# Optimization experiments

Hardware: AMD Instinct MI355X
Metric: run time of the kernel (lower is better)

The kernel has to match this reference:

```python
import jax, jax.numpy as jnp
import numpy as np
import math

NUM_HEADS = 16
D_MODEL = 1024
HEAD_DIM = D_MODEL // NUM_HEADS


def setup_inputs() -> dict:
    key = jax.random.key(0)
    k1, k2, k3 = jax.random.split(key, 3)
    x = jax.random.normal(k1, (4, 2048, D_MODEL), dtype=jnp.float32)
    # Linear(d_model, 3*d_model, bias=False): y = x @ w_qkv, w_qkv: [d_model, 3*d_model]
    w_qkv = jax.random.normal(k2, (D_MODEL, 3 * D_MODEL), dtype=jnp.float32) * (1.0 / math.sqrt(D_MODEL))
    w_o = jax.random.normal(k3, (D_MODEL, D_MODEL), dtype=jnp.float32) * (1.0 / math.sqrt(D_MODEL))
    return {"x": x, "w_qkv": w_qkv, "w_o": w_o}


def reference(x, w_qkv, w_o):
    B, S, _ = x.shape
    H, Dh = NUM_HEADS, HEAD_DIM
    qkv = (x @ w_qkv).reshape(B, S, 3, H, Dh)
    q = qkv[:, :, 0].transpose(0, 2, 1, 3)  # [B, H, S, Dh]
    k = qkv[:, :, 1].transpose(0, 2, 1, 3)
    v = qkv[:, :, 2].transpose(0, 2, 1, 3)
    scale = 1.0 / math.sqrt(Dh + 1e-9)
    scores = jnp.einsum("bhqd,bhkd->bhqk", q, k) * scale  # [B, H, S, S]
    probs = jax.nn.softmax(scores, axis=-1)
    # dropout is identity in eval mode
    out = jnp.einsum("bhqk,bhkd->bhqd", probs, v)  # [B, H, S, Dh]
    out = out.transpose(0, 2, 1, 3).reshape(B, S, H * Dh)
    return out @ w_o
```

## Files before the change

kernel.cpp:

```cpp
#include <hip/hip_runtime.h>
#include <hip/hip_bf16.h>

typedef __bf16 bf16_t;
typedef __bf16 bf16x8 __attribute__((ext_vector_type(8)));
typedef float f32x4 __attribute__((ext_vector_type(4)));
typedef unsigned int uint32x2 __attribute__((ext_vector_type(2)));
typedef unsigned int uint32x4 __attribute__((ext_vector_type(4)));

#define B_SZ 4
#define SEQ 2048
#define NH 16
#define DH 64
#define DM 1024
#define RSQ (3 * DM)

__device__ __forceinline__ void gload_lds16(const bf16_t* g, bf16_t* l) {
  __builtin_amdgcn_global_load_lds(
      (const __attribute__((address_space(1))) unsigned int*)g,
      (__attribute__((address_space(3))) unsigned int*)l, 16, 0, 0);
}

__device__ __forceinline__ unsigned lds_b32addr(void* p) {
  return (unsigned)(uintptr_t)(__attribute__((address_space(3))) void*)p;
}

__global__ __launch_bounds__(256) void f32_to_bf16_kernel(
    const float* __restrict__ in, bf16_t* __restrict__ out, int n) {
  int i = (blockIdx.x * blockDim.x + threadIdx.x) * 4;
  if (i >= n) return;
  float4 v = *reinterpret_cast<const float4*>(in + i);
  bf16_t o[4] = {(bf16_t)v.x, (bf16_t)v.y, (bf16_t)v.z, (bf16_t)v.w};
  *reinterpret_cast<uint2*>(out + i) = *reinterpret_cast<const uint2*>(o);
}

__global__ __launch_bounds__(256) void transpose_f32_bf16_kernel(
    const float* __restrict__ in, bf16_t* __restrict__ outT, int K, int N,
    int scale_cols, float scale) {
  __shared__ float tile[32][33];
  const int tx = threadIdx.x & 31;
  const int ty = threadIdx.x >> 5;
  const int n0 = blockIdx.x * 32;
  const int k0 = blockIdx.y * 32;
#pragma unroll
  for (int j = 0; j < 4; ++j)
    tile[ty + j * 8][tx] = in[(size_t)(k0 + ty + j * 8) * N + n0 + tx];
  __syncthreads();
#pragma unroll
  for (int j = 0; j < 4; ++j) {
    int n = n0 + ty + j * 8;
    float s = (n < scale_cols) ? scale : 1.0f;
    outT[(size_t)n * K + k0 + tx] = (bf16_t)(tile[tx][ty + j * 8] * s);
  }
}

template <typename OutT>
__global__ __launch_bounds__(512, 2) void gemm8p_kernel(
    const bf16_t* __restrict__ A, const bf16_t* __restrict__ Bt,
    OutT* __restrict__ C, int M, int N, int K, int NB) {
  __shared__ __align__(16) bf16_t As[2][128 * 64];
  __shared__ __align__(16) bf16_t Bs[2][256 * 64];

  const int tid = threadIdx.x;
  const int lane = tid & 63;
  const int wid = tid >> 6;
  const int l16 = lane & 15;
  const int g4 = lane >> 4;
  const int wm = wid >> 2;
  const int wn = wid & 3;
  const int tiles = K >> 6;

  const int nwg = gridDim.x;
  const int bid = blockIdx.x;
  const int swz = (bid & 7) * (nwg >> 3) + (bid >> 3);
  const int m0 = (swz / NB) * 128;
  const int n0 = (swz % NB) * 256;

  const bf16_t* aglob = A + (size_t)(m0 + (tid >> 3)) * K + (tid & 7) * 8;

  auto stageA = [&](int t) {
    int tt = (t == tiles) ? 0 : t;
    int k0 = tt * 64;
    int buf = tt & 1;
#pragma unroll
    for (int i = 0; i < 2; ++i)
      gload_lds16(aglob + (size_t)i * 64 * K + k0,
                  &As[buf][i * 4096 + wid * 512]);
  };
  auto stageB = [&](int t, int h) {
    int tt = (t == tiles) ? 0 : t;
    int k0 = tt * 64;
    int buf = tt & 1;
#pragma unroll
    for (int j = 0; j < 2; ++j) {
      int wrow = (2 * j + (wid >> 2)) * 64 + (wid & 3) * 8 + h * 32;
      gload_lds16(
          Bt + (size_t)(n0 + wrow + (lane >> 3)) * K + k0 + (lane & 7) * 8,
          &Bs[buf][wrow * 64]);
    }
  };

  f32x4 acc[4][4] = {};

  stageA(0);
  stageB(0, 0);
  stageB(0, 1);
  asm volatile("s_waitcnt vmcnt(2)" ::: "memory");
  __builtin_amdgcn_s_barrier();
  __builtin_amdgcn_sched_barrier(0);

#pragma unroll 2
  for (int t = 0; t < tiles; ++t) {
    const int buf = t & 1;
    const int abase = (wm * 64 + l16) * 64 + g4 * 8;
    const int bbase = (wn * 64 + l16) * 64 + g4 * 8;

    bf16x8 af[4][2], bf[2][2];
#pragma unroll
    for (int m = 0; m < 4; ++m)
#pragma unroll
      for (int ks = 0; ks < 2; ++ks)
        af[m][ks] = *reinterpret_cast<const bf16x8*>(
            &As[buf][abase + m * 16 * 64 + ks * 32]);
#pragma unroll
    for (int n = 0; n < 2; ++n)
#pragma unroll
      for (int ks = 0; ks < 2; ++ks)
        bf[n][ks] = *reinterpret_cast<const bf16x8*>(
            &Bs[buf][bbase + n * 16 * 64 + ks * 32]);

    stageA(t + 1);
    stageB(t + 1, 0);
    asm volatile("s_waitcnt vmcnt(4)" ::: "memory");
    __builtin_amdgcn_s_barrier();
    __builtin_amdgcn_sched_barrier(0);

    __builtin_amdgcn_s_setprio(1);
#pragma unroll
    for (int m = 0; m < 4; ++m)
#pragma unroll
      for (int n = 0; n < 2; ++n)
#pragma unroll
        for (int ks = 0; ks < 2; ++ks)
          acc[m][n] = __builtin_amdgcn_mfma_f32_16x16x32_bf16(
              af[m][ks], bf[n][ks], acc[m][n], 0, 0, 0);
    __builtin_amdgcn_s_setprio(0);
    __builtin_amdgcn_s_barrier();
    __builtin_amdgcn_sched_barrier(0);

    bf16x8 bg[2][2];
#pragma unroll
    for (int n = 0; n < 2; ++n)
#pragma unroll
      for (int ks = 0; ks < 2; ++ks)
        bg[n][ks] = *reinterpret_cast<const bf16x8*>(
            &Bs[buf][bbase + (n + 2) * 16 * 64 + ks * 32]);

    stageB(t + 1, 1);
    asm volatile("s_waitcnt vmcnt(2)" ::: "memory");
    __builtin_amdgcn_s_barrier();
    __builtin_amdgcn_sched_barrier(0);

    __builtin_amdgcn_s_setprio(1);
#pragma unroll
    for (int m = 0; m < 4; ++m)
#pragma unroll
      for (int n = 0; n < 2; ++n)
#pragma unroll
        for (int ks = 0; ks < 2; ++ks)
          acc[m][n + 2] = __builtin_amdgcn_mfma_f32_16x16x32_bf16(
              af[m][ks], bg[n][ks], acc[m][n + 2], 0, 0, 0);
    __builtin_amdgcn_s_setprio(0);
    __builtin_amdgcn_s_barrier();
    __builtin_amdgcn_sched_barrier(0);
  }

  asm volatile("s_waitcnt vmcnt(0)" ::: "memory");

#pragma unroll
  for (int m = 0; m < 4; ++m)
#pragma unroll
    for (int n = 0; n < 4; ++n)
#pragma unroll
      for (int r = 0; r < 4; ++r) {
        int row = m0 + wm * 64 + m * 16 + g4 * 4 + r;
        int col = n0 + wn * 64 + n * 16 + l16;
        C[(size_t)row * N + col] = (OutT)acc[m][n][r];
      }
}

template <bool PRE>
__device__ __forceinline__ void attn_body(
    const bf16_t* kp, const bf16_t* vp_next, bf16_t* vst_next, unsigned vrd,
    const bf16x8 (&qf)[4][2], f32x4 (&acc_o)[16], float (&lsum)[4]) {
  uint32x4 kf[2][2];
#pragma unroll
  for (int half = 0; half < 2; ++half)
#pragma unroll
    for (int kh = 0; kh < 2; ++kh)
      asm volatile("global_load_dwordx4 %0, %1, off"
                   : "=v"(kf[half][kh])
                   : "v"(kp + (size_t)half * 64 * RSQ + kh * 32)
                   : "memory");

  if constexpr (PRE) {
#pragma unroll
    for (int t = 0; t < 4; ++t)
      gload_lds16(vp_next + t * 16, vst_next + t * 512);
  }

  if constexpr (PRE)
    asm volatile("s_waitcnt vmcnt(8)" ::: "memory");
  else
    asm volatile("s_waitcnt vmcnt(4)" ::: "memory");

  uint32x2 vr[4][2];
#define TRR(dst, OFFSTR)                              \
  asm volatile("ds_read_b64_tr_b16 %0, %1 offset:" OFFSTR \
               : "=v"(dst)                            \
               : "v"(vrd))
  TRR(vr[0][0], "0");    TRR(vr[0][1], "512");
  TRR(vr[1][0], "1024"); TRR(vr[1][1], "1536");
  TRR(vr[2][0], "2048"); TRR(vr[2][1], "2560");
  TRR(vr[3][0], "3072"); TRR(vr[3][1], "3584");
#undef TRR

  if constexpr (PRE)
    asm volatile("s_waitcnt vmcnt(4)" ::: "memory");
  else
    asm volatile("s_waitcnt vmcnt(0)" ::: "memory");
  __builtin_amdgcn_sched_barrier(0);

  f32x4 sA[4] = {}, sB[4] = {};
#pragma unroll
  for (int qb = 0; qb < 4; ++qb) {
    sA[qb] = __builtin_amdgcn_mfma_f32_16x16x32_bf16(
        __builtin_bit_cast(bf16x8, kf[0][0]), qf[qb][0], sA[qb], 0, 0, 0);
    sA[qb] = __builtin_amdgcn_mfma_f32_16x16x32_bf16(
        __builtin_bit_cast(bf16x8, kf[0][1]), qf[qb][1], sA[qb], 0, 0, 0);
    sB[qb] = __builtin_amdgcn_mfma_f32_16x16x32_bf16(
        __builtin_bit_cast(bf16x8, kf[1][0]), qf[qb][0], sB[qb], 0, 0, 0);
    sB[qb] = __builtin_amdgcn_mfma_f32_16x16x32_bf16(
        __builtin_bit_cast(bf16x8, kf[1][1]), qf[qb][1], sB[qb], 0, 0, 0);
  }

  bf16x8 pf[4];
#pragma unroll
  for (int qb = 0; qb < 4; ++qb) {
    float p0 = __builtin_amdgcn_exp2f(sA[qb][0]);
    float p1 = __builtin_amdgcn_exp2f(sA[qb][1]);
    float p2 = __builtin_amdgcn_exp2f(sA[qb][2]);
    float p3 = __builtin_amdgcn_exp2f(sA[qb][3]);
    float p4 = __builtin_amdgcn_exp2f(sB[qb][0]);
    float p5 = __builtin_amdgcn_exp2f(sB[qb][1]);
    float p6 = __builtin_amdgcn_exp2f(sB[qb][2]);
    float p7 = __builtin_amdgcn_exp2f(sB[qb][3]);
    lsum[qb] += ((p0 + p1) + (p2 + p3)) + ((p4 + p5) + (p6 + p7));
    pf[qb][0] = (bf16_t)p0; pf[qb][1] = (bf16_t)p1;
    pf[qb][2] = (bf16_t)p2; pf[qb][3] = (bf16_t)p3;
    pf[qb][4] = (bf16_t)p4; pf[qb][5] = (bf16_t)p5;
    pf[qb][6] = (bf16_t)p6; pf[qb][7] = (bf16_t)p7;
  }

  asm volatile("s_waitcnt lgkmcnt(0)" ::: "memory");
  __builtin_amdgcn_sched_barrier(0);
  bf16x8 vf[4];
#pragma unroll
  for (int db = 0; db < 4; ++db) {
    uint32x4 c = {vr[db][0].x, vr[db][0].y, vr[db][1].x, vr[db][1].y};
    vf[db] = __builtin_bit_cast(bf16x8, c);
  }
#pragma unroll
  for (int qb = 0; qb < 4; ++qb)
#pragma unroll
    for (int db = 0; db < 4; ++db)
      acc_o[qb * 4 + db] = __builtin_amdgcn_mfma_f32_16x16x32_bf16(
          pf[qb], vf[db], acc_o[qb * 4 + db], 0, 0, 0);
}

__global__ __launch_bounds__(256) void attn_kernel(
    const bf16_t* __restrict__ qkv, bf16_t* __restrict__ out) {
  __shared__ __align__(16) unsigned char smem[33792];
  bf16_t* Vlds = (bf16_t*)smem;
  float(*Obuf)[66] = (float(*)[66])smem;
  float* lbuf = (float*)(smem + 32768);

  const int tid = threadIdx.x;
  const int lane = tid & 63;
  const int wid = tid >> 6;
  const int l16 = lane & 15;
  const int g4 = lane >> 4;

  const int D = blockIdx.x;
  const int g = ((D >> 8) << 3) + (D & 7);
  const int h = g & 15;
  const int b = g >> 4;
  const int q0 = ((D >> 3) & 31) * 64;

  const size_t base = (size_t)b * SEQ * RSQ;

  bf16x8 qf[4][2];
#pragma unroll
  for (int qb = 0; qb < 4; ++qb)
#pragma unroll
    for (int kh = 0; kh < 2; ++kh)
      qf[qb][kh] = __builtin_bit_cast(
          bf16x8, *reinterpret_cast<const uint4*>(
                      qkv + base + (size_t)(q0 + qb * 16 + l16) * RSQ + h * DH +
                      kh * 32 + g4 * 8));

  const bf16_t* kbase =
      qkv + base + (size_t)(wid * 16 + l16) * RSQ + DM + h * DH + g4 * 8;

  const int keyoff = ((lane >> 5) << 6) + wid * 16 + (((lane >> 3) & 3) << 2) +
                     ((lane >> 1) & 3);
  const bf16_t* vsrc =
      qkv + base + (size_t)keyoff * RSQ + 2 * DM + h * DH + (lane & 1) * 8;
  bf16_t* vwave = Vlds + wid * 4096;
  const unsigned vlane = lds_b32addr(vwave) + (lane << 3);

  f32x4 acc_o[16] = {};
  float lsum[4] = {0.f, 0.f, 0.f, 0.f};

#pragma unroll
  for (int t = 0; t < 4; ++t) gload_lds16(vsrc + t * 16, vwave + t * 512);

  for (int i = 0; i < 15; ++i) {
    const bf16_t* kp = kbase + (size_t)i * 128 * RSQ;
    const bf16_t* vp_next = vsrc + (size_t)(i + 1) * 128 * RSQ;
    bf16_t* vst_next = vwave + ((i + 1) & 1) * 2048;
    unsigned vrd = vlane + (i & 1) * 4096;
    attn_body<true>(kp, vp_next, vst_next, vrd, qf, acc_o, lsum);
  }
  attn_body<false>(kbase + (size_t)15 * 128 * RSQ, nullptr, nullptr,
                   vlane + 4096, qf, acc_o, lsum);

#pragma unroll
  for (int qb = 0; qb < 4; ++qb) {
    float t = lsum[qb];
    t += __shfl_xor(t, 16, 64);
    t += __shfl_xor(t, 32, 64);
    if (g4 == 0) lbuf[wid * 64 + qb * 16 + l16] = t;
  }

  for (int ph = 0; ph < 4; ++ph) {
    __syncthreads();
    if (wid == ph) {
#pragma unroll
      for (int qb = 0; qb < 4; ++qb)
#pragma unroll
        for (int db = 0; db < 4; ++db)
#pragma unroll
          for (int r = 0; r < 4; ++r) {
            int q = qb * 16 + g4 * 4 + r;
            int d = db * 16 + l16;
            if (ph == 0)
              Obuf[q][d] = acc_o[qb * 4 + db][r];
            else
              Obuf[q][d] += acc_o[qb * 4 + db][r];
          }
    }
  }
  __syncthreads();

  {
    int q = wid * 16 + l16;
    float l = lbuf[0 * 64 + q] + lbuf[1 * 64 + q] + lbuf[2 * 64 + q] +
              lbuf[3 * 64 + q];
    float inv = 1.f / l;
    bf16_t ob[16];
#pragma unroll
    for (int c = 0; c < 16; ++c)
      ob[c] = (bf16_t)(Obuf[q][g4 * 16 + c] * inv);
    bf16_t* op = out + (size_t)(b * SEQ + q0 + q) * DM + h * DH + g4 * 16;
    *reinterpret_cast<uint4*>(op) = *reinterpret_cast<const uint4*>(&ob[0]);
    *reinterpret_cast<uint4*>(op + 8) = *reinterpret_cast<const uint4*>(&ob[8]);
  }
}

extern "C" void kernel_launch(void* const* d_in, const int* in_sizes, int n_in,
                              void* d_out, int out_size, void* d_ws, size_t ws_size,
                              hipStream_t stream) {
  const float* x = (const float*)d_in[0];
  const float* w_qkv = (const float*)d_in[1];
  const float* w_o = (const float*)d_in[2];
  float* out = (float*)d_out;

  bf16_t* xb = (bf16_t*)d_ws;
  bf16_t* wqkvt = xb + (size_t)8192 * 1024;
  bf16_t* wot = wqkvt + (size_t)3072 * 1024;
  bf16_t* qkv = wot + (size_t)1024 * 1024;
  bf16_t* attn = qkv + (size_t)8192 * 3072;

  const float c_exp2 = 0.18033688011112042f;

  f32_to_bf16_kernel<<<8192, 256, 0, stream>>>(x, xb, 8192 * 1024);
  transpose_f32_bf16_kernel<<<dim3(3072 / 32, 1024 / 32), 256, 0, stream>>>(
      w_qkv, wqkvt, 1024, 3072, 1024, c_exp2);
  transpose_f32_bf16_kernel<<<dim3(1024 / 32, 1024 / 32), 256, 0, stream>>>(
      w_o, wot, 1024, 1024, 0, 1.0f);

  gemm8p_kernel<bf16_t><<<768, 512, 0, stream>>>(
      xb, wqkvt, qkv, 8192, 3072, 1024, 12);
  attn_kernel<<<2048, 256, 0, stream>>>(qkv, attn);
  gemm8p_kernel<float><<<256, 512, 0, stream>>>(
      attn, wot, out, 8192, 1024, 1024, 4);
}
```

Before: 233.5 us.

## Triple-buffer GEMM with XOR-swizzled LDS and one barrier per K tile

New measurement: 223.5 us. 4.3% less time.

```diff
diff --git a/kernel.cpp b/kernel.cpp
--- a/kernel.cpp
+++ b/kernel.cpp
@@ -54,11 +54,11 @@
 }
 
 template <typename OutT>
-__global__ __launch_bounds__(512, 2) void gemm8p_kernel(
+__global__ __launch_bounds__(512, 2) void gemm_dp_kernel(
     const bf16_t* __restrict__ A, const bf16_t* __restrict__ Bt,
     OutT* __restrict__ C, int M, int N, int K, int NB) {
-  __shared__ __align__(16) bf16_t As[2][128 * 64];
-  __shared__ __align__(16) bf16_t Bs[2][256 * 64];
+  __shared__ __align__(16) bf16_t As[3][128 * 64];
+  __shared__ __align__(16) bf16_t Bs[3][256 * 64];
 
   const int tid = threadIdx.x;
   const int lane = tid & 63;
@@ -75,106 +75,73 @@
   const int m0 = (swz / NB) * 128;
   const int n0 = (swz % NB) * 256;
 
-  const bf16_t* aglob = A + (size_t)(m0 + (tid >> 3)) * K + (tid & 7) * 8;
-
-  auto stageA = [&](int t) {
-    int tt = (t == tiles) ? 0 : t;
-    int k0 = tt * 64;
-    int buf = tt & 1;
+  const int srow = tid >> 3;
+  const int scol = ((tid & 7) ^ (srow & 7)) * 8;
+  const bf16_t* aglob = A + (size_t)(m0 + srow) * K + scol;
+  const bf16_t* bglob = Bt + (size_t)(n0 + srow) * K + scol;
+
+  auto stage = [&](int t) {
+    const int buf = t % 3;
+    const int k0 = t * 64;
 #pragma unroll
     for (int i = 0; i < 2; ++i)
       gload_lds16(aglob + (size_t)i * 64 * K + k0,
                   &As[buf][i * 4096 + wid * 512]);
+#pragma unroll
+    for (int j = 0; j < 4; ++j)
+      gload_lds16(bglob + (size_t)j * 64 * K + k0,
+                  &Bs[buf][j * 4096 + wid * 512]);
   };
-  auto stageB = [&](int t, int h) {
-    int tt = (t == tiles) ? 0 : t;
-    int k0 = tt * 64;
-    int buf = tt & 1;
-#pragma unroll
-    for (int j = 0; j < 2; ++j) {
-      int wrow = (2 * j + (wid >> 2)) * 64 + (wid & 3) * 8 + h * 32;
-      gload_lds16(
-          Bt + (size_t)(n0 + wrow + (lane >> 3)) * K + k0 + (lane & 7) * 8,
-          &Bs[buf][wrow * 64]);
-    }
-  };
 
   f32x4 acc[4][4] = {};
 
-  stageA(0);
-  stageB(0, 0);
-  stageB(0, 1);
-  asm volatile("s_waitcnt vmcnt(2)" ::: "memory");
+  stage(0);
+  stage(1);
+  asm volatile("s_waitcnt vmcnt(6)" ::: "memory");
   __builtin_amdgcn_s_barrier();
   __builtin_amdgcn_sched_barrier(0);
 
-#pragma unroll 2
+  const int xr = l16 & 7;
+
   for (int t = 0; t < tiles; ++t) {
-    const int buf = t & 1;
-    const int abase = (wm * 64 + l16) * 64 + g4 * 8;
-    const int bbase = (wn * 64 + l16) * 64 + g4 * 8;
-
-    bf16x8 af[4][2], bf[2][2];
+    const int buf = t % 3;
+
+    bf16x8 af[4][2], bff[4][2];
 #pragma unroll
     for (int m = 0; m < 4; ++m)
 #pragma unroll
       for (int ks = 0; ks < 2; ++ks)
         af[m][ks] = *reinterpret_cast<const bf16x8*>(
-            &As[buf][abase + m * 16 * 64 + ks * 32]);
-#pragma unroll
-    for (int n = 0; n < 2; ++n)
+            &As[buf][(wm * 64 + m * 16 + l16) * 64 +
+                     ((ks * 4 + g4) ^ xr) * 8]);
+#pragma unroll
+    for (int n = 0; n < 4; ++n)
 #pragma unroll
       for (int ks = 0; ks < 2; ++ks)
-        bf[n][ks] = *reinterpret_cast<const bf16x8*>(
-            &Bs[buf][bbase + n * 16 * 64 + ks * 32]);
-
-    stageA(t + 1);
-    stageB(t + 1, 0);
-    asm volatile("s_waitcnt vmcnt(4)" ::: "memory");
+        bff[n][ks] = *reinterpret_cast<const bf16x8*>(
+            &Bs[buf][(wn * 64 + n * 16 + l16) * 64 +
+                     ((ks * 4 + g4) ^ xr) * 8]);
+
+    if (t + 2 < tiles) stage(t + 2);
+
+    __builtin_amdgcn_s_setprio(1);
+#pragma unroll
+    for (int m = 0; m < 4; ++m)
+#pragma unroll
+      for (int n = 0; n < 4; ++n)
+#pragma unroll
+        for (int ks = 0; ks < 2; ++ks)
+          acc[m][n] = __builtin_amdgcn_mfma_f32_16x16x32_bf16(
+              af[m][ks], bff[n][ks], acc[m][n], 0, 0, 0);
+    __builtin_amdgcn_s_setprio(0);
+
+    if (t + 2 < tiles)
+      asm volatile("s_waitcnt vmcnt(6)" ::: "memory");
+    else
+      asm volatile("s_waitcnt vmcnt(0)" ::: "memory");
     __builtin_amdgcn_s_barrier();
     __builtin_amdgcn_sched_barrier(0);
-
-    __builtin_amdgcn_s_setprio(1);
-#pragma unroll
-    for (int m = 0; m < 4; ++m)
-#pragma unroll
-      for (int n = 0; n < 2; ++n)
-#pragma unroll
-        for (int ks = 0; ks < 2; ++ks)
-          acc[m][n] = __builtin_amdgcn_mfma_f32_16x16x32_bf16(
-              af[m][ks], bf[n][ks], acc[m][n], 0, 0, 0);
-    __builtin_amdgcn_s_setprio(0);
-    __builtin_amdgcn_s_barrier();
-    __builtin_amdgcn_sched_barrier(0);
-
-    bf16x8 bg[2][2];
-#pragma unroll
-    for (int n = 0; n < 2; ++n)
-#pragma unroll
-      for (int ks = 0; ks < 2; ++ks)
-        bg[n][ks] = *reinterpret_cast<const bf16x8*>(
-            &Bs[buf][bbase + (n + 2) * 16 * 64 + ks * 32]);
-
-    stageB(t + 1, 1);
-    asm volatile("s_waitcnt vmcnt(2)" ::: "memory");
-    __builtin_amdgcn_s_barrier();
-    __builtin_amdgcn_sched_barrier(0);
-
-    __builtin_amdgcn_s_setprio(1);
-#pragma unroll
-    for (int m = 0; m < 4; ++m)
-#pragma unroll
-      for (int n = 0; n < 2; ++n)
-#pragma unroll
-        for (int ks = 0; ks < 2; ++ks)
-          acc[m][n + 2] = __builtin_amdgcn_mfma_f32_16x16x32_bf16(
-              af[m][ks], bg[n][ks], acc[m][n + 2], 0, 0, 0);
-    __builtin_amdgcn_s_setprio(0);
-    __builtin_amdgcn_s_barrier();
-    __builtin_amdgcn_sched_barrier(0);
-  }
-
-  asm volatile("s_waitcnt vmcnt(0)" ::: "memory");
+  }
 
 #pragma unroll
   for (int m = 0; m < 4; ++m)
@@ -399,9 +366,9 @@
   transpose_f32_bf16_kernel<<<dim3(1024 / 32, 1024 / 32), 256, 0, stream>>>(
       w_o, wot, 1024, 1024, 0, 1.0f);
 
-  gemm8p_kernel<bf16_t><<<768, 512, 0, stream>>>(
+  gemm_dp_kernel<bf16_t><<<768, 512, 0, stream>>>(
       xb, wqkvt, qkv, 8192, 3072, 1024, 12);
   attn_kernel<<<2048, 256, 0, stream>>>(qkv, attn);
-  gemm8p_kernel<float><<<256, 512, 0, stream>>>(
+  gemm_dp_kernel<float><<<256, 512, 0, stream>>>(
       attn, wot, out, 8192, 1024, 1024, 4);
 }
```
